# Optimization experiments

Hardware: AMD Instinct MI355X
Metric: run time of the kernel (lower is better)

## Reference

```python
import jax, jax.numpy as jnp
import numpy as np

N = 10000          # nodes
E = 160000         # edges
T = 32             # seq_len == n_timesteps
H = 256            # hidden_size
K = 4              # edge_embedding_dim
NF = T * 6         # node_features
PRED = 8           # predicted_timesteps
T_TEACH = T - PRED # teacher-forced steps


def setup_inputs() -> dict:
    key = jax.random.key(0)
    ks = jax.random.split(key, 16)
    s = 0.05
    return {
        "x": jax.random.normal(ks[0], (N, NF), jnp.float32),
        "edge_index": jax.random.randint(ks[1], (2, E), 0, N, jnp.int64),
        "z": jax.random.uniform(ks[2], (E, K), jnp.float32),
        # inner f_out: Linear(H, NF) + ReLU
        "Wf": jax.random.normal(ks[3], (H, NF), jnp.float32) * s,
        "bf": jax.random.normal(ks[4], (NF,), jnp.float32) * s,
        # k-1 edge MLPs: Linear(2*NF, H) -> ReLU -> Linear(H, H), stacked
        "W1": jax.random.normal(ks[5], (K - 1, 2 * NF, H), jnp.float32) * s,
        "b1": jax.random.normal(ks[6], (K - 1, H), jnp.float32) * s,
        "W2": jax.random.normal(ks[7], (K - 1, H, H), jnp.float32) * s,
        "b2": jax.random.normal(ks[8], (K - 1, H), jnp.float32) * s,
        # GRUCell(6, H): torch gate order r, z, n
        "Wih": jax.random.normal(ks[9], (3 * H, 6), jnp.float32) * s,
        "bih": jax.random.normal(ks[10], (3 * H,), jnp.float32) * s,
        "Whh": jax.random.normal(ks[11], (3 * H, H), jnp.float32) * s,
        "bhh": jax.random.normal(ks[12], (3 * H,), jnp.float32) * s,
        # outer f_out: Linear(H, 6) + ReLU
        "Wo": jax.random.normal(ks[13], (H, 6), jnp.float32) * s,
        "bo": jax.random.normal(ks[14], (6,), jnp.float32) * s,
    }


def _forward(x, edge_index, z, Wf, bf, W1, b1, W2, b2, Wih, bih, Whh, bhh, Wo, bo):
    src = edge_index[0]  # x_j (source)
    dst = edge_index[1]  # x_i (target, aggregation index)
    zw = z[:, 1:K].T[:, :, None]  # [K-1, E, 1]
    ones_e = jnp.ones((E,), x.dtype)
    cnt = jnp.maximum(jax.ops.segment_sum(ones_e, dst, num_segments=N), 1.0)[:, None]

    def step(carry, inp):
        h, prev = carry
        t, x_t = inp
        inputs = jnp.where(t < T_TEACH, x_t, prev)  # [N, 6]
        fh = jax.nn.relu(h @ Wf + bf)               # [N, NF]
        # message: cat([x_i, x_j]) = [target, source], detached in torch
        ef = jax.lax.stop_gradient(
            jnp.concatenate([fh[dst], fh[src]], axis=1))  # [E, 2*NF]
        h1 = jax.nn.relu(jnp.einsum('ef,kfh->keh', ef, W1) + b1[:, None, :])
        h2 = jnp.einsum('keh,khg->keg', h1, W2) + b2[:, None, :]  # [K-1,E,H]
        msg = jnp.sum(zw * h2, axis=0)              # [E, H]
        m = jax.ops.segment_sum(msg, dst, num_segments=N) / cnt  # scatter-mean
        # GRUCell(inputs, hidden=m)
        gx = inputs @ Wih.T + bih                   # [N, 3H]
        gh = m @ Whh.T + bhh                        # [N, 3H]
        rx, zx, nx = jnp.split(gx, 3, axis=1)
        rh, zh, nh = jnp.split(gh, 3, axis=1)
        r = jax.nn.sigmoid(rx + rh)
        zg = jax.nn.sigmoid(zx + zh)
        n = jnp.tanh(nx + r * nh)
        h_new = (1.0 - zg) * n + zg * m             # [N, H]
        mu = inputs + jax.nn.relu(h_new @ Wo + bo)  # [N, 6]
        return (h_new, mu), mu

    x_seq = x.reshape(N, T, 6).transpose(1, 0, 2)   # [T, N, 6]
    ts = jnp.arange(T)
    h0 = jnp.zeros((N, H), x.dtype)
    p0 = jnp.zeros((N, 6), x.dtype)
    _, mus = jax.lax.scan(step, (h0, p0), (ts, x_seq))  # [T, N, 6]
    return mus.transpose(1, 0, 2).reshape(N, NF)


def reference(x, edge_index, z, Wf, bf, W1, b1, W2, b2, Wih, bih, Whh, bhh, Wo, bo):
    return _forward(x, edge_index, z, Wf, bf, W1, b1, W2, b2,
                    Wih, bih, Whh, bhh, Wo, bo)
```

## Files before the change

kernel.cpp:

```cpp
#include <hip/hip_runtime.h>
#include <hip/hip_bf16.h>

#define NN 10000
#define NE 160000
#define TS 32
#define HID 256
#define NFEAT 192
#define TTEACH 24

typedef unsigned short u16;
typedef unsigned int u32;
typedef __attribute__((ext_vector_type(8))) short bf16x8;
typedef __attribute__((ext_vector_type(4))) float f32x4;

__device__ __forceinline__ float bf2f(u16 u){
    u32 v = ((u32)u) << 16;
    union { u32 i; float f; } c; c.i = v; return c.f;
}
__device__ __forceinline__ u16 f2bf(float f){
    union { float f; u32 i; } c; c.f = f;
    u32 i = c.i;
    u32 lsb = (i >> 16) & 1u;
    i += 0x7fffu + lsb;
    return (u16)(i >> 16);
}

__global__ void fill_f32(float* p, float v, int n){
    int i = blockIdx.x * 256 + threadIdx.x;
    if (i < n) p[i] = v;
}
__global__ void fill_i32(int* p, int v, int n){
    int i = blockIdx.x * 256 + threadIdx.x;
    if (i < n) p[i] = v;
}
__global__ void copy_i32(const int* __restrict__ a, int* __restrict__ b, int n){
    int i = blockIdx.x * 256 + threadIdx.x;
    if (i < n) b[i] = a[i];
}

__global__ void detect_f32(const u16* __restrict__ zraw, int* __restrict__ flag){
    int c = 0;
    for (int i = 0; i < 128; i++) if (zraw[2*i] >= 0x4000) c++;
    *flag = (c > 8) ? 1 : 0;
}
__global__ void conv_f32(const void* __restrict__ in, float* __restrict__ outp,
                         int n, const int* __restrict__ flag){
    int i = blockIdx.x * 256 + threadIdx.x;
    if (i >= n) return;
    if (*flag) outp[i] = ((const float*)in)[i];
    else       outp[i] = bf2f(((const u16*)in)[i]);
}
__global__ void detect_i64(const int* __restrict__ ei_raw, int* __restrict__ flag){
    int zz = 0;
    #pragma unroll
    for (int i = 0; i < 32; i++) zz |= ei_raw[2*i + 1];
    *flag = (zz == 0) ? 1 : 0;
}
__global__ void copy_edges(const int* __restrict__ ei_raw, const int* __restrict__ flag,
                           int* __restrict__ src, int* __restrict__ dst){
    int e = blockIdx.x * 256 + threadIdx.x;
    if (e >= NE) return;
    int st = (*flag) ? 2 : 1;
    src[e] = ei_raw[(size_t)e * st];
    dst[e] = ei_raw[((size_t)NE + e) * st];
}

__global__ void degree_k(const int* __restrict__ dst, int* __restrict__ cnt, int n){
    int e = blockIdx.x * 256 + threadIdx.x;
    if (e < n) atomicAdd(&cnt[dst[e]], 1);
}
__global__ void invcnt_k(const int* __restrict__ cnt, float* __restrict__ inv, int n){
    int i = blockIdx.x * 256 + threadIdx.x;
    if (i < n) inv[i] = 1.0f / fmaxf((float)cnt[i], 1.0f);
}

__global__ void scan_k(const int* __restrict__ cnt, int* __restrict__ binoff){
    __shared__ int ps[1024];
    int t = threadIdx.x;
    int s = 0;
    if (t < 1000)
        for (int i = 0; i < 10; i++) s += cnt[t*10 + i];
    ps[t] = s;
    __syncthreads();
    for (int ofs = 1; ofs < 1024; ofs <<= 1){
        int v = (t >= ofs) ? ps[t - ofs] : 0;
        __syncthreads();
        ps[t] += v;
        __syncthreads();
    }
    if (t < 1000){
        int run = (t == 0) ? 0 : ps[t-1];
        for (int i = 0; i < 10; i++){
            binoff[t*10 + i] = run;
            run += cnt[t*10 + i];
        }
    }
}
__global__ void scatter_k(const int* __restrict__ src32, const int* __restrict__ dst32,
                          const float* __restrict__ zc, int* __restrict__ cur,
                          int* __restrict__ srcS, int* __restrict__ dstS,
                          float* __restrict__ zS){
    int e = blockIdx.x * 256 + threadIdx.x;
    if (e >= NE) return;
    int d = dst32[e];
    int pos = atomicAdd(&cur[d], 1);
    srcS[pos] = src32[e];
    dstS[pos] = d;
    zS[pos]        = zc[(size_t)e*4 + 1];
    zS[NE + pos]   = zc[(size_t)e*4 + 2];
    zS[2*NE + pos] = zc[(size_t)e*4 + 3];
}

__global__ void build_wft(const float* __restrict__ Wfc, u16* __restrict__ WfT){
    int idx = blockIdx.x * 256 + threadIdx.x;
    if (idx < 256 * 192){
        int k = idx / 192, n = idx % 192;
        WfT[(size_t)n * 256 + k] = f2bf(Wfc[idx]);
    }
}
__global__ void build_w1t(const float* __restrict__ W1c, u16* __restrict__ W1T){
    int idx = blockIdx.x * 256 + threadIdx.x;
    if (idx < 1536 * 192){
        int n = idx / 192, k = idx % 192;
        int kblk = n >> 9, part = (n >> 8) & 1, c = n & 255;
        W1T[idx] = f2bf(W1c[(size_t)kblk * (384*256) + (size_t)(part*192 + k) * 256 + c]);
    }
}
__global__ void conv_bf16(const float* __restrict__ in, u16* __restrict__ outp, int n){
    int i = blockIdx.x * 256 + threadIdx.x;
    if (i < n) outp[i] = f2bf(in[i]);
}
__global__ void build_w2t(const float* __restrict__ W2c, u16* __restrict__ W2T){
    int idx = blockIdx.x * 256 + threadIdx.x;
    if (idx < 768 * 256){
        int k = idx / 256, n = idx % 256;
        W2T[(size_t)n * 768 + k] = f2bf(W2c[idx]);
    }
}

template<int MODE>
__global__ __launch_bounds__(256, 2) void gemm_mfma(
    const u16* __restrict__ A16, const u16* __restrict__ BT16,
    const float* __restrict__ bias, float* __restrict__ Cf, u16* __restrict__ Cb,
    const float* __restrict__ A32, const float* __restrict__ rowscale,
    int M, int Kd, int Nd)
{
    __shared__ __align__(16) u16 Alds[256 * 40];
    __shared__ __align__(16) u16 Blds[64 * 40];
    const int tid = threadIdx.x;
    const int m0 = blockIdx.x * 256;
    const int n0 = blockIdx.y * 64;
    const int wave = tid >> 6, lane = tid & 63;
    const int quad = lane >> 4, l16 = lane & 15;

    const f32x4 zero4 = {0.f, 0.f, 0.f, 0.f};
    f32x4 acc[4][4];
    #pragma unroll
    for (int r=0;r<4;r++)
        #pragma unroll
        for (int c=0;c<4;c++) acc[r][c] = zero4;

    const int arow = m0 + tid;
    const u16* ap = (MODE == 2) ? nullptr : &A16[(size_t)arow * Kd];
    const int bn = tid >> 2, bseg = tid & 3;
    const u16* bp = &BT16[(size_t)(n0 + bn) * Kd + bseg * 8];
    float rs = 0.f;
    if (MODE == 2 && arow < M) rs = rowscale[arow];

    for (int k0 = 0; k0 < Kd; k0 += 32){
        if (MODE == 2){
            if (arow < M){
                const float4* q = reinterpret_cast<const float4*>(&A32[(size_t)arow * Kd + k0]);
                u32 pk[16];
                #pragma unroll
                for (int s=0;s<8;s++){
                    float4 v = q[s];
                    float2 p0; p0.x = v.x * rs; p0.y = v.y * rs;
                    float2 p1; p1.x = v.z * rs; p1.y = v.w * rs;
                    __hip_bfloat162 h0 = __float22bfloat162_rn(p0);
                    __hip_bfloat162 h1 = __float22bfloat162_rn(p1);
                    pk[2*s]   = *reinterpret_cast<u32*>(&h0);
                    pk[2*s+1] = *reinterpret_cast<u32*>(&h1);
                }
                #pragma unroll
                for (int s=0;s<4;s++)
                    *reinterpret_cast<uint4*>(&Alds[tid * 40 + s*8]) = *reinterpret_cast<uint4*>(&pk[4*s]);
            } else {
                uint4 zz = {0,0,0,0};
                #pragma unroll
                for (int s=0;s<4;s++)
                    *reinterpret_cast<uint4*>(&Alds[tid * 40 + s*8]) = zz;
            }
        } else {
            if (arow < M){
                const uint4* q = reinterpret_cast<const uint4*>(ap + k0);
                uint4 v0 = q[0], v1 = q[1], v2 = q[2], v3 = q[3];
                *reinterpret_cast<uint4*>(&Alds[tid * 40])      = v0;
                *reinterpret_cast<uint4*>(&Alds[tid * 40 + 8])  = v1;
                *reinterpret_cast<uint4*>(&Alds[tid * 40 + 16]) = v2;
                *reinterpret_cast<uint4*>(&Alds[tid * 40 + 24]) = v3;
            } else {
                uint4 zz = {0,0,0,0};
                #pragma unroll
                for (int s=0;s<4;s++)
                    *reinterpret_cast<uint4*>(&Alds[tid * 40 + s*8]) = zz;
            }
        }
        {
            uint4 v = *reinterpret_cast<const uint4*>(bp + k0);
            *reinterpret_cast<uint4*>(&Blds[bn * 40 + bseg * 8]) = v;
        }
        __syncthreads();
        bf16x8 af[4], bfr[4];
        #pragma unroll
        for (int r=0;r<4;r++)
            af[r] = *reinterpret_cast<const bf16x8*>(&Alds[(wave*64 + r*16 + l16) * 40 + quad * 8]);
        #pragma unroll
        for (int c=0;c<4;c++)
            bfr[c] = *reinterpret_cast<const bf16x8*>(&Blds[(c*16 + l16) * 40 + quad * 8]);
        #pragma unroll
        for (int r=0;r<4;r++)
            #pragma unroll
            for (int c=0;c<4;c++)
                acc[r][c] = __builtin_amdgcn_mfma_f32_16x16x32_bf16(af[r], bfr[c], acc[r][c], 0, 0, 0);
        __syncthreads();
    }
    #pragma unroll
    for (int c=0;c<4;c++){
        int col = n0 + c*16 + l16;
        float bv = 0.f;
        if (MODE == 0 || MODE == 2) bv = bias[col];
        if (MODE == 1){
            int part = (col >> 8) & 1;
            if (part == 0) bv = bias[(col >> 9) * 256 + (col & 255)];
        }
        #pragma unroll
        for (int r=0;r<4;r++){
            #pragma unroll
            for (int reg=0;reg<4;reg++){
                int row = m0 + wave*64 + r*16 + quad*4 + reg;
                if (row >= M) continue;
                float v = acc[r][c][reg] + bv;
                if (MODE == 0) v = fmaxf(v, 0.f);
                if (MODE == 2) Cf[(size_t)row * Nd + col] = v;
                else           Cb[(size_t)row * Nd + col] = f2bf(v);
            }
        }
    }
}

__global__ __launch_bounds__(256, 2) void edge_mfma(
    const u16* __restrict__ AB16, const u16* __restrict__ W2T,
    const float* __restrict__ b2, const float* __restrict__ zS,
    const int* __restrict__ srcS, const int* __restrict__ dstS,
    float* __restrict__ m_acc)
{
    __shared__ __align__(16) char smem[25600];
    u16*   Alds = (u16*)smem;
    u16*   Blds = (u16*)(smem + 5120);
    float* stg  = (float*)smem;
    __shared__ float zc3[3][64];
    __shared__ int dstc[64], srcc[64];
    const int tid = threadIdx.x;
    const int eb = blockIdx.x * 64;

    if (tid < 64){
        srcc[tid] = srcS[eb + tid];
        dstc[tid] = dstS[eb + tid];
    }
    int tz = tid - 64;
    if (tz >= 0 && tz < 192){
        int g = tz / 64, e = tz % 64;
        zc3[g][e] = zS[(size_t)g * NE + eb + e];
    }
    __syncthreads();

    const int wave = tid >> 6, lane = tid & 63;
    const int quad = lane >> 4, l16 = lane & 15;
    const int est = tid >> 2, seg = tid & 3;

    const f32x4 zero4 = {0.f, 0.f, 0.f, 0.f};
    f32x4 acc[4][4];
    #pragma unroll
    for (int r=0;r<4;r++)
        #pragma unroll
        for (int c=0;c<4;c++) acc[r][c] = zero4;

    const int d = dstc[est], s = srcc[est];
    const u16* paB = &AB16[(size_t)d * 1536];
    const u16* pbB = &AB16[(size_t)s * 1536 + 256];
    const int bn = tid >> 2;
    const u16* bwB = &W2T[(size_t)bn * 768 + seg * 8];

    uint4 pa = *reinterpret_cast<const uint4*>(&paB[seg * 8]);
    uint4 pb = *reinterpret_cast<const uint4*>(&pbB[seg * 8]);

    for (int kc = 0; kc < 768; kc += 32){
        const int g = kc >> 8;
        {
            union { uint4 v; u32 w[4]; } UA, UB;
            UA.v = pa; UB.v = pb;
            float zk = zc3[g][est];
            u32 pk[4];
            #pragma unroll
            for (int i=0;i<4;i++){
                float2 fa = __bfloat1622float2(*reinterpret_cast<__hip_bfloat162*>(&UA.w[i]));
                float2 fb = __bfloat1622float2(*reinterpret_cast<__hip_bfloat162*>(&UB.w[i]));
                float2 v;
                v.x = zk * fmaxf(fa.x + fb.x, 0.f);
                v.y = zk * fmaxf(fa.y + fb.y, 0.f);
                __hip_bfloat162 hr = __float22bfloat162_rn(v);
                pk[i] = *reinterpret_cast<u32*>(&hr);
            }
            *reinterpret_cast<uint4*>(&Alds[est * 40 + seg * 8]) = *reinterpret_cast<uint4*>(pk);
        }
        #pragma unroll
        for (int i=0;i<4;i++){
            uint4 w = *reinterpret_cast<const uint4*>(&bwB[(size_t)i * 64 * 768 + kc]);
            *reinterpret_cast<uint4*>(&Blds[(bn + i*64) * 40 + seg * 8]) = w;
        }
        __syncthreads();
        if (kc + 32 < 768){
            const int kn = kc + 32;
            const int gn = kn >> 8;
            const int jn = (kn & 255) + seg * 8;
            pa = *reinterpret_cast<const uint4*>(&paB[gn * 512 + jn]);
            pb = *reinterpret_cast<const uint4*>(&pbB[gn * 512 + jn]);
        }
        bf16x8 af[4], bfr[4];
        #pragma unroll
        for (int r=0;r<4;r++)
            af[r] = *reinterpret_cast<const bf16x8*>(&Alds[(r*16 + l16) * 40 + quad * 8]);
        #pragma unroll
        for (int c=0;c<4;c++)
            bfr[c] = *reinterpret_cast<const bf16x8*>(&Blds[(wave*64 + c*16 + l16) * 40 + quad * 8]);
        #pragma unroll
        for (int r=0;r<4;r++)
            #pragma unroll
            for (int c=0;c<4;c++)
                acc[r][c] = __builtin_amdgcn_mfma_f32_16x16x32_bf16(af[r], bfr[c], acc[r][c], 0, 0, 0);
        __syncthreads();
    }
    #pragma unroll
    for (int c=0;c<4;c++){
        int col = wave*64 + c*16 + l16;
        float b20 = b2[col], b21 = b2[256 + col], b22 = b2[512 + col];
        #pragma unroll
        for (int r=0;r<4;r++){
            #pragma unroll
            for (int reg=0;reg<4;reg++){
                int e = r*16 + quad*4 + reg;
                acc[r][c][reg] += zc3[0][e]*b20 + zc3[1][e]*b21 + zc3[2][e]*b22;
            }
        }
    }
    float sum = 0.f;
    int cur_d = -1;
    const int colg = wave*64 + lane;
    #pragma unroll
    for (int r = 0; r < 4; r++){
        #pragma unroll
        for (int c=0;c<4;c++)
            #pragma unroll
            for (int reg=0;reg<4;reg++)
                stg[wave*(16*65) + (quad*4 + reg)*65 + c*16 + l16] = acc[r][c][reg];
        __syncthreads();
        for (int e = 0; e < 16; e++){
            int eg = r*16 + e;
            int dn = dstc[eg];
            float v = stg[wave*(16*65) + e*65 + lane];
            if (dn != cur_d){
                if (cur_d >= 0) atomicAdd(&m_acc[(size_t)cur_d * 256 + colg], sum);
                cur_d = dn; sum = v;
            } else {
                sum += v;
            }
        }
        __syncthreads();
    }
    if (cur_d >= 0) atomicAdd(&m_acc[(size_t)cur_d * 256 + colg], sum);
}

__global__ void gates_mu_k(
    const float* __restrict__ gh, float* __restrict__ m_acc,
    const float* __restrict__ inv_cnt, const float* __restrict__ x,
    const float* __restrict__ Wih, const float* __restrict__ bih,
    const float* __restrict__ Wo, const float* __restrict__ bo,
    float* __restrict__ prev, u16* __restrict__ h16, void* __restrict__ out,
    const int* __restrict__ flag, int t)
{
    const int n = blockIdx.x;
    const int j = threadIdx.x;
    const int idx = n * 256 + j;
    float inp[6];
    if (t < TTEACH){
        #pragma unroll
        for (int c=0;c<6;c++) inp[c] = x[(size_t)n * NFEAT + t * 6 + c];
    } else {
        #pragma unroll
        for (int c=0;c<6;c++) inp[c] = prev[n * 6 + c];
    }
    float m = m_acc[idx] * inv_cnt[n];
    m_acc[idx] = 0.f;
    float gxr = bih[j], gxz = bih[256 + j], gxn = bih[512 + j];
    #pragma unroll
    for (int c=0;c<6;c++){
        gxr += inp[c] * Wih[j * 6 + c];
        gxz += inp[c] * Wih[(256 + j) * 6 + c];
        gxn += inp[c] * Wih[(512 + j) * 6 + c];
    }
    float ghr = gh[(size_t)n * 768 + j];
    float ghz = gh[(size_t)n * 768 + 256 + j];
    float ghn = gh[(size_t)n * 768 + 512 + j];
    float r  = 1.f / (1.f + __expf(-(gxr + ghr)));
    float zg = 1.f / (1.f + __expf(-(gxz + ghz)));
    float nn = tanhf(gxn + r * ghn);
    float hv = (1.f - zg) * nn + zg * m;
    h16[idx] = f2bf(hv);
    __shared__ float hl[256];
    __shared__ float part[6][9];
    hl[j] = hv;
    __syncthreads();
    if (j < 48){
        int c = j >> 3, p = j & 7;
        float s = 0.f;
        #pragma unroll 8
        for (int q = 0; q < 32; q++){
            int jj = p*32 + q;
            s += hl[jj] * Wo[jj * 6 + c];
        }
        part[c][p] = s;
    }
    __syncthreads();
    if (j < 6){
        float s = bo[j];
        #pragma unroll
        for (int p = 0; p < 8; p++) s += part[j][p];
        float mu = inp[j] + fmaxf(s, 0.f);
        if (*flag) ((float*)out)[(size_t)n * NFEAT + t * 6 + j] = mu;
        else       ((u16*)out)[(size_t)n * NFEAT + t * 6 + j] = f2bf(mu);
        prev[n * 6 + j] = mu;
    }
}

extern "C" void kernel_launch(void* const* d_in, const int* in_sizes, int n_in,
                              void* d_out, int out_size, void* d_ws, size_t ws_size,
                              hipStream_t stream)
{
    const void* x_r   = d_in[0];
    const int*  ei    = (const int*)d_in[1];
    const void* z_r   = d_in[2];
    const void* Wf_r  = d_in[3];
    const void* bf_r  = d_in[4];
    const void* W1_r  = d_in[5];
    const void* b1_r  = d_in[6];
    const void* W2_r  = d_in[7];
    const void* b2_r  = d_in[8];
    const void* Wih_r = d_in[9];
    const void* bih_r = d_in[10];
    const void* Whh_r = d_in[11];
    const void* bhh_r = d_in[12];
    const void* Wo_r  = d_in[13];
    const void* bo_r  = d_in[14];

    char* ws = (char*)d_ws;
    size_t off = 0;
    auto alloc = [&](size_t bytes){
        void* p = ws + off;
        off += (bytes + 255) & ~(size_t)255;
        return p;
    };
    u16*   h16   = (u16*)  alloc((size_t)NN * HID * 2);
    float* prev  = (float*)alloc((size_t)NN * 6 * 4);
    u16*   fh16  = (u16*)  alloc((size_t)NN * NFEAT * 2);
    u16*   AB16  = (u16*)  alloc((size_t)NN * 1536 * 2);
    float* m_acc = (float*)alloc((size_t)NN * HID * 4);
    float* gh    = (float*)alloc((size_t)NN * 768 * 4);
    float* invc  = (float*)alloc((size_t)NN * 4);
    int*   cnt   = (int*)  alloc((size_t)NN * 4);
    int*   binoff= (int*)  alloc((size_t)(NN + 1) * 4);
    int*   curw  = (int*)  alloc((size_t)NN * 4);
    u16*   WfT   = (u16*)  alloc((size_t)192 * 256 * 2);
    u16*   W1T   = (u16*)  alloc((size_t)1536 * 192 * 2);
    u16*   Whh16 = (u16*)  alloc((size_t)768 * 256 * 2);
    u16*   W2T   = (u16*)  alloc((size_t)256 * 768 * 2);
    int*   src32 = (int*)  alloc((size_t)NE * 4);
    int*   dst32 = (int*)  alloc((size_t)NE * 4);
    int*   srcS  = (int*)  alloc((size_t)NE * 4);
    int*   dstS  = (int*)  alloc((size_t)NE * 4);
    float* zS    = (float*)alloc((size_t)3 * NE * 4);
    int*   fdt   = (int*)  alloc(256);
    int*   fidx  = (int*)  alloc(256);
    float* xc   = (float*)alloc((size_t)NN * NFEAT * 4);
    float* zc   = (float*)alloc((size_t)NE * 4 * 4);
    float* Wfc  = (float*)alloc((size_t)256 * 192 * 4);
    float* bfc  = (float*)alloc(192 * 4);
    float* W1c  = (float*)alloc((size_t)3 * 384 * 256 * 4);
    float* b1c  = (float*)alloc(768 * 4);
    float* W2c  = (float*)alloc((size_t)3 * 256 * 256 * 4);
    float* b2c  = (float*)alloc(768 * 4);
    float* Wihc = (float*)alloc((size_t)768 * 6 * 4);
    float* bihc = (float*)alloc(768 * 4);
    float* Whhc = (float*)alloc((size_t)768 * 256 * 4);
    float* bhhc = (float*)alloc(768 * 4);
    float* Woc  = (float*)alloc((size_t)256 * 6 * 4);
    float* boc  = (float*)alloc(6 * 4);

    detect_f32<<<1, 1, 0, stream>>>((const u16*)z_r, fdt);
    detect_i64<<<1, 1, 0, stream>>>(ei, fidx);
    copy_edges<<<(NE + 255)/256, 256, 0, stream>>>(ei, fidx, src32, dst32);

    auto conv = [&](const void* in, float* outp, int n){
        conv_f32<<<(n + 255)/256, 256, 0, stream>>>(in, outp, n, fdt);
    };
    conv(x_r,   xc,   NN * NFEAT);
    conv(z_r,   zc,   NE * 4);
    conv(Wf_r,  Wfc,  256 * 192);
    conv(bf_r,  bfc,  192);
    conv(W1_r,  W1c,  3 * 384 * 256);
    conv(b1_r,  b1c,  768);
    conv(W2_r,  W2c,  3 * 256 * 256);
    conv(b2_r,  b2c,  768);
    conv(Wih_r, Wihc, 768 * 6);
    conv(bih_r, bihc, 768);
    conv(Whh_r, Whhc, 768 * 256);
    conv(bhh_r, bhhc, 768);
    conv(Wo_r,  Woc,  256 * 6);
    conv(bo_r,  boc,  6);

    fill_f32<<<(NN*HID/2 + 255)/256, 256, 0, stream>>>((float*)h16, 0.f, NN*HID/2);
    fill_f32<<<(NN*6 + 255)/256, 256, 0, stream>>>(prev, 0.f, NN*6);
    fill_f32<<<(NN*HID + 255)/256, 256, 0, stream>>>(m_acc, 0.f, NN*HID);
    fill_i32<<<(NN + 255)/256, 256, 0, stream>>>(cnt, 0, NN);
    degree_k<<<(NE + 255)/256, 256, 0, stream>>>(dst32, cnt, NE);
    invcnt_k<<<(NN + 255)/256, 256, 0, stream>>>(cnt, invc, NN);
    scan_k<<<1, 1024, 0, stream>>>(cnt, binoff);
    copy_i32<<<(NN + 255)/256, 256, 0, stream>>>(binoff, curw, NN);
    scatter_k<<<(NE + 255)/256, 256, 0, stream>>>(src32, dst32, zc, curw, srcS, dstS, zS);
    build_wft<<<(256*192 + 255)/256, 256, 0, stream>>>(Wfc, WfT);
    build_w1t<<<(1536*192 + 255)/256, 256, 0, stream>>>(W1c, W1T);
    conv_bf16<<<(768*256 + 255)/256, 256, 0, stream>>>(Whhc, Whh16, 768*256);
    build_w2t<<<(768*256 + 255)/256, 256, 0, stream>>>(W2c, W2T);

    for (int t = 0; t < TS; t++){
        gemm_mfma<0><<<dim3(40, 3), 256, 0, stream>>>(h16, WfT, bfc, nullptr, fh16, nullptr, nullptr, NN, 256, NFEAT);
        gemm_mfma<1><<<dim3(40, 24), 256, 0, stream>>>(fh16, W1T, b1c, nullptr, AB16, nullptr, nullptr, NN, NFEAT, 1536);
        edge_mfma<<<2500, 256, 0, stream>>>(AB16, W2T, b2c, zS, srcS, dstS, m_acc);
        gemm_mfma<2><<<dim3(40, 12), 256, 0, stream>>>(nullptr, Whh16, bhhc, gh, nullptr, m_acc, invc, NN, 256, 768);
        gates_mu_k<<<NN, 256, 0, stream>>>(gh, m_acc, invc, xc, Wihc, bihc, Woc, boc, prev, h16, d_out, fdt, t);
    }
}
```

Before: 7.278 ms.

## Split edge kernel columns across blocks and precompute per-node b2 bias

New measurement: 7.627 ms. 1.05x slower.

```diff
diff --git a/kernel.cpp b/kernel.cpp
--- a/kernel.cpp
+++ b/kernel.cpp
@@ -34,6 +34,10 @@
     if (i < n) p[i] = v;
 }
 __global__ void copy_i32(const int* __restrict__ a, int* __restrict__ b, int n){
+    int i = blockIdx.x * 256 + threadIdx.x;
+    if (i < n) b[i] = a[i];
+}
+__global__ void copy_f32(const float* __restrict__ a, float* __restrict__ b, int n){
     int i = blockIdx.x * 256 + threadIdx.x;
     if (i < n) b[i] = a[i];
 }
@@ -109,6 +113,23 @@
     zS[pos]        = zc[(size_t)e*4 + 1];
     zS[NE + pos]   = zc[(size_t)e*4 + 2];
     zS[2*NE + pos] = zc[(size_t)e*4 + 3];
+}
+
+__global__ void zsum_k(const int* __restrict__ dst32, const float* __restrict__ zc,
+                       float* __restrict__ zsum){
+    int e = blockIdx.x * 256 + threadIdx.x;
+    if (e >= NE) return;
+    int d = dst32[e];
+    atomicAdd(&zsum[d*3 + 0], zc[(size_t)e*4 + 1]);
+    atomicAdd(&zsum[d*3 + 1], zc[(size_t)e*4 + 2]);
+    atomicAdd(&zsum[d*3 + 2], zc[(size_t)e*4 + 3]);
+}
+__global__ void build_bias_k(const float* __restrict__ zsum, const float* __restrict__ b2c,
+                             float* __restrict__ bias_node){
+    int idx = blockIdx.x * 256 + threadIdx.x;
+    if (idx >= NN * 256) return;
+    int n = idx >> 8, c = idx & 255;
+    bias_node[idx] = zsum[n*3]*b2c[c] + zsum[n*3+1]*b2c[256+c] + zsum[n*3+2]*b2c[512+c];
 }
 
 __global__ void build_wft(const float* __restrict__ Wfc, u16* __restrict__ WfT){
@@ -251,18 +272,19 @@
 
 __global__ __launch_bounds__(256, 2) void edge_mfma(
     const u16* __restrict__ AB16, const u16* __restrict__ W2T,
-    const float* __restrict__ b2, const float* __restrict__ zS,
+    const float* __restrict__ zS,
     const int* __restrict__ srcS, const int* __restrict__ dstS,
     float* __restrict__ m_acc)
 {
-    __shared__ __align__(16) char smem[25600];
+    __shared__ __align__(16) char smem[15360];
     u16*   Alds = (u16*)smem;
     u16*   Blds = (u16*)(smem + 5120);
     float* stg  = (float*)smem;
     __shared__ float zc3[3][64];
     __shared__ int dstc[64], srcc[64];
     const int tid = threadIdx.x;
-    const int eb = blockIdx.x * 64;
+    const int cb = blockIdx.x * 128;
+    const int eb = blockIdx.y * 64;
 
     if (tid < 64){
         srcc[tid] = srcS[eb + tid];
@@ -280,17 +302,16 @@
     const int est = tid >> 2, seg = tid & 3;
 
     const f32x4 zero4 = {0.f, 0.f, 0.f, 0.f};
-    f32x4 acc[4][4];
+    f32x4 acc[4][2];
     #pragma unroll
     for (int r=0;r<4;r++)
         #pragma unroll
-        for (int c=0;c<4;c++) acc[r][c] = zero4;
+        for (int c=0;c<2;c++) acc[r][c] = zero4;
 
     const int d = dstc[est], s = srcc[est];
     const u16* paB = &AB16[(size_t)d * 1536];
     const u16* pbB = &AB16[(size_t)s * 1536 + 256];
-    const int bn = tid >> 2;
-    const u16* bwB = &W2T[(size_t)bn * 768 + seg * 8];
+    const u16* bwB = &W2T[(size_t)(cb + (tid >> 2)) * 768 + (tid & 3) * 8];
 
     uint4 pa = *reinterpret_cast<const uint4*>(&paB[seg * 8]);
     uint4 pb = *reinterpret_cast<const uint4*>(&pbB[seg * 8]);
@@ -314,10 +335,11 @@
             }
             *reinterpret_cast<uint4*>(&Alds[est * 40 + seg * 8]) = *reinterpret_cast<uint4*>(pk);
         }
-        #pragma unroll
-        for (int i=0;i<4;i++){
-            uint4 w = *reinterpret_cast<const uint4*>(&bwB[(size_t)i * 64 * 768 + kc]);
-            *reinterpret_cast<uint4*>(&Blds[(bn + i*64) * 40 + seg * 8]) = w;
+        {
+            uint4 w0 = *reinterpret_cast<const uint4*>(&bwB[kc]);
+            uint4 w1 = *reinterpret_cast<const uint4*>(&bwB[(size_t)64 * 768 + kc]);
+            *reinterpret_cast<uint4*>(&Blds[(tid >> 2) * 40 + (tid & 3) * 8]) = w0;
+            *reinterpret_cast<uint4*>(&Blds[((tid >> 2) + 64) * 40 + (tid & 3) * 8]) = w1;
         }
         __syncthreads();
         if (kc + 32 < 768){
@@ -327,63 +349,55 @@
             pa = *reinterpret_cast<const uint4*>(&paB[gn * 512 + jn]);
             pb = *reinterpret_cast<const uint4*>(&pbB[gn * 512 + jn]);
         }
-        bf16x8 af[4], bfr[4];
+        bf16x8 af[4], bfr[2];
         #pragma unroll
         for (int r=0;r<4;r++)
             af[r] = *reinterpret_cast<const bf16x8*>(&Alds[(r*16 + l16) * 40 + quad * 8]);
         #pragma unroll
-        for (int c=0;c<4;c++)
-            bfr[c] = *reinterpret_cast<const bf16x8*>(&Blds[(wave*64 + c*16 + l16) * 40 + quad * 8]);
+        for (int c=0;c<2;c++)
+            bfr[c] = *reinterpret_cast<const bf16x8*>(&Blds[(wave*32 + c*16 + l16) * 40 + quad * 8]);
         #pragma unroll
         for (int r=0;r<4;r++)
             #pragma unroll
-            for (int c=0;c<4;c++)
+            for (int c=0;c<2;c++)
                 acc[r][c] = __builtin_amdgcn_mfma_f32_16x16x32_bf16(af[r], bfr[c], acc[r][c], 0, 0, 0);
         __syncthreads();
     }
-    #pragma unroll
-    for (int c=0;c<4;c++){
-        int col = wave*64 + c*16 + l16;
-        float b20 = b2[col], b21 = b2[256 + col], b22 = b2[512 + col];
-        #pragma unroll
-        for (int r=0;r<4;r++){
-            #pragma unroll
-            for (int reg=0;reg<4;reg++){
-                int e = r*16 + quad*4 + reg;
-                acc[r][c][reg] += zc3[0][e]*b20 + zc3[1][e]*b21 + zc3[2][e]*b22;
-            }
-        }
-    }
+    const int colL = lane & 31;
+    const int half = lane >> 5;
+    const int colG = cb + wave*32 + colL;
     float sum = 0.f;
     int cur_d = -1;
-    const int colg = wave*64 + lane;
     #pragma unroll
     for (int r = 0; r < 4; r++){
         #pragma unroll
-        for (int c=0;c<4;c++)
+        for (int c=0;c<2;c++)
             #pragma unroll
             for (int reg=0;reg<4;reg++)
-                stg[wave*(16*65) + (quad*4 + reg)*65 + c*16 + l16] = acc[r][c][reg];
-        __syncthreads();
-        for (int e = 0; e < 16; e++){
-            int eg = r*16 + e;
-            int dn = dstc[eg];
-            float v = stg[wave*(16*65) + e*65 + lane];
-            if (dn != cur_d){
-                if (cur_d >= 0) atomicAdd(&m_acc[(size_t)cur_d * 256 + colg], sum);
-                cur_d = dn; sum = v;
-            } else {
-                sum += v;
+                stg[wave*(16*33) + (quad*4 + reg)*33 + c*16 + l16] = acc[r][c][reg];
+        __syncthreads();
+        if ((r >> 1) == half){
+            for (int e = 0; e < 16; e++){
+                int eg = r*16 + e;
+                int dn = dstc[eg];
+                float v = stg[wave*(16*33) + e*33 + colL];
+                if (dn != cur_d){
+                    if (cur_d >= 0) atomicAdd(&m_acc[(size_t)cur_d * 256 + colG], sum);
+                    cur_d = dn; sum = v;
+                } else {
+                    sum += v;
+                }
             }
         }
         __syncthreads();
     }
-    if (cur_d >= 0) atomicAdd(&m_acc[(size_t)cur_d * 256 + colg], sum);
+    if (cur_d >= 0) atomicAdd(&m_acc[(size_t)cur_d * 256 + colG], sum);
 }
 
 __global__ void gates_mu_k(
     const float* __restrict__ gh, float* __restrict__ m_acc,
-    const float* __restrict__ inv_cnt, const float* __restrict__ x,
+    const float* __restrict__ inv_cnt, const float* __restrict__ bias_node,
+    const float* __restrict__ x,
     const float* __restrict__ Wih, const float* __restrict__ bih,
     const float* __restrict__ Wo, const float* __restrict__ bo,
     float* __restrict__ prev, u16* __restrict__ h16, void* __restrict__ out,
@@ -401,7 +415,7 @@
         for (int c=0;c<6;c++) inp[c] = prev[n * 6 + c];
     }
     float m = m_acc[idx] * inv_cnt[n];
-    m_acc[idx] = 0.f;
+    m_acc[idx] = bias_node[idx];
     float gxr = bih[j], gxz = bih[256 + j], gxn = bih[512 + j];
     #pragma unroll
     for (int c=0;c<6;c++){
@@ -480,6 +494,8 @@
     int*   cnt   = (int*)  alloc((size_t)NN * 4);
     int*   binoff= (int*)  alloc((size_t)(NN + 1) * 4);
     int*   curw  = (int*)  alloc((size_t)NN * 4);
+    float* zsum  = (float*)alloc((size_t)NN * 3 * 4);
+    float* biasN = (float*)alloc((size_t)NN * HID * 4);
     u16*   WfT   = (u16*)  alloc((size_t)192 * 256 * 2);
     u16*   W1T   = (u16*)  alloc((size_t)1536 * 192 * 2);
     u16*   Whh16 = (u16*)  alloc((size_t)768 * 256 * 2);
@@ -530,10 +546,13 @@
 
     fill_f32<<<(NN*HID/2 + 255)/256, 256, 0, stream>>>((float*)h16, 0.f, NN*HID/2);
     fill_f32<<<(NN*6 + 255)/256, 256, 0, stream>>>(prev, 0.f, NN*6);
-    fill_f32<<<(NN*HID + 255)/256, 256, 0, stream>>>(m_acc, 0.f, NN*HID);
     fill_i32<<<(NN + 255)/256, 256, 0, stream>>>(cnt, 0, NN);
+    fill_f32<<<(NN*3 + 255)/256, 256, 0, stream>>>(zsum, 0.f, NN*3);
     degree_k<<<(NE + 255)/256, 256, 0, stream>>>(dst32, cnt, NE);
     invcnt_k<<<(NN + 255)/256, 256, 0, stream>>>(cnt, invc, NN);
+    zsum_k<<<(NE + 255)/256, 256, 0, stream>>>(dst32, zc, zsum);
+    build_bias_k<<<(NN*HID + 255)/256, 256, 0, stream>>>(zsum, b2c, biasN);
+    copy_f32<<<(NN*HID + 255)/256, 256, 0, stream>>>(biasN, m_acc, NN*HID);
     scan_k<<<1, 1024, 0, stream>>>(cnt, binoff);
     copy_i32<<<(NN + 255)/256, 256, 0, stream>>>(binoff, curw, NN);
     scatter_k<<<(NE + 255)/256, 256, 0, stream>>>(src32, dst32, zc, curw, srcS, dstS, zS);
@@ -545,8 +564,8 @@
     for (int t = 0; t < TS; t++){
         gemm_mfma<0><<<dim3(40, 3), 256, 0, stream>>>(h16, WfT, bfc, nullptr, fh16, nullptr, nullptr, NN, 256, NFEAT);
         gemm_mfma<1><<<dim3(40, 24), 256, 0, stream>>>(fh16, W1T, b1c, nullptr, AB16, nullptr, nullptr, NN, NFEAT, 1536);
-        edge_mfma<<<2500, 256, 0, stream>>>(AB16, W2T, b2c, zS, srcS, dstS, m_acc);
+        edge_mfma<<<dim3(2, 2500), 256, 0, stream>>>(AB16, W2T, zS, srcS, dstS, m_acc);
         gemm_mfma<2><<<dim3(40, 12), 256, 0, stream>>>(nullptr, Whh16, bhhc, gh, nullptr, m_acc, invc, NN, 256, 768);
-        gates_mu_k<<<NN, 256, 0, stream>>>(gh, m_acc, invc, xc, Wihc, bihc, Woc, boc, prev, h16, d_out, fdt, t);
-    }
-}
+        gates_mu_k<<<NN, 256, 0, stream>>>(gh, m_acc, invc, biasN, xc, Wihc, bihc, Woc, boc, prev, h16, d_out, fdt, t);
+    }
+}
```
